# Kernel optimization log

Measured on AMD Instinct MI355X. Metric: run time of the kernel, lower is better.

## Reference

```python
import jax, jax.numpy as jnp
import numpy as np

B, DIM, N, K, NA = 1, 64, 1024, 16, 12
POS_HID = 64
ATTN_HID = 4 * DIM


def setup_inputs() -> dict:
    key = jax.random.key(0)
    ks = jax.random.split(key, 8)
    s = 0.05  # small init scale, mimics xavier magnitude
    return {
        "xyz": jax.random.normal(ks[0], (B, 3, N), jnp.float32),
        "feats": jax.random.normal(ks[1], (B, DIM, N, NA), jnp.float32),
        "anchors": jax.random.normal(ks[2], (NA, 3, 3), jnp.float32),
        "to_qkv": jax.random.normal(ks[3], (3 * DIM, DIM), jnp.float32) * s,
        "pos_mlp1": jax.random.normal(ks[4], (POS_HID, 3), jnp.float32) * s,
        "pos_mlp2": jax.random.normal(ks[5], (DIM, POS_HID), jnp.float32) * s,
        "attn_mlp1": jax.random.normal(ks[6], (ATTN_HID, DIM), jnp.float32) * s,
        "attn_mlp2": jax.random.normal(ks[7], (DIM, ATTN_HID), jnp.float32) * s,
    }


def reference(xyz, feats, anchors, to_qkv, pos_mlp1, pos_mlp2, attn_mlp1, attn_mlp2):
    # --- KNN over points (self included) ---
    pts = jnp.swapaxes(xyz, 1, 2)                      # [B,N,3]
    sq = jnp.sum(pts * pts, axis=-1)                   # [B,N]
    d2 = sq[:, :, None] + sq[:, None, :] - 2.0 * jnp.einsum('bnd,bmd->bnm', pts, pts)
    _, idx = jax.lax.top_k(-d2, K)                     # [B,N,K] nearest indices

    # --- gather helpers (vmapped over batch) ---
    gather3 = jax.vmap(lambda x, i: x[:, i])           # [C,N],[N,K] -> [C,N,K]
    gather4 = jax.vmap(lambda x, i: x[:, i, :])        # [C,N,A],[N,K] -> [C,N,K,A]

    # --- relative positions rotated by anchors ---
    grouped_xyz = gather3(xyz, idx)                    # [B,3,N,K]
    rel = xyz[:, :, :, None] - grouped_xyz             # [B,3,N,K]
    gx = jnp.einsum('aij,bjnk->binka', anchors, rel)   # [B,3,N,K,NA]

    # --- positional embedding MLP ---
    pe = jnp.einsum('ji,binka->bjnka', pos_mlp1, gx)   # [B,POS_HID,N,K,NA]
    pe = jax.nn.relu(pe)
    pe = jnp.einsum('ji,binka->bjnka', pos_mlp2, pe)   # [B,DIM,N,K,NA]

    # --- qkv projection ---
    qkv = jnp.einsum('ji,bina->bjna', to_qkv, feats)   # [B,3*DIM,N,NA]
    q, k, v = jnp.split(qkv, 3, axis=1)                # each [B,DIM,N,NA]

    k_g = gather4(k, idx)                              # [B,DIM,N,K,NA]
    v_g = gather4(v, idx) + pe                         # [B,DIM,N,K,NA]
    qk_rel = q[:, :, :, None, :] - k_g                 # [B,DIM,N,K,NA]

    # --- attention MLP on (qk_rel + pe) ---
    sim = qk_rel + pe
    sim = jnp.einsum('ji,binka->bjnka', attn_mlp1, sim)  # [B,4*DIM,N,K,NA]
    sim = jax.nn.relu(sim)
    sim = jnp.einsum('ji,binka->bjnka', attn_mlp2, sim)  # [B,DIM,N,K,NA]

    # --- per-channel softmax over neighbor axis, aggregate ---
    attn = jax.nn.softmax(sim, axis=-2)
    return jnp.sum(attn * v_g, axis=-2)                # [B,DIM,N,NA]
```

## Files before the change

### kernel.cpp

```cpp
#include <hip/hip_runtime.h>

#define NPTS 1024
#define DIM 64
#define KNN 16
#define NA 12
#define NCOL 192

typedef __attribute__((ext_vector_type(8))) short bf16x8;
typedef __attribute__((ext_vector_type(4))) float f32x4;

static __device__ inline unsigned short f2bfu(float x) {
    __bf16 b = (__bf16)x;
    return __builtin_bit_cast(unsigned short, b);
}
static __device__ inline float bf2f(unsigned short s) {
    return __uint_as_float(((unsigned)s) << 16);
}
static __device__ inline unsigned pk2(float lo, float hi) {
    return (unsigned)f2bfu(lo) | ((unsigned)f2bfu(hi) << 16);
}
static __device__ inline bf16x8 load8_cvt(const float* p) {
    f32x4 u = *(const f32x4*)p;
    f32x4 v = *(const f32x4*)(p + 4);
    bf16x8 r;
    r[0] = (short)f2bfu(u[0]); r[1] = (short)f2bfu(u[1]); r[2] = (short)f2bfu(u[2]); r[3] = (short)f2bfu(u[3]);
    r[4] = (short)f2bfu(v[0]); r[5] = (short)f2bfu(v[1]); r[6] = (short)f2bfu(v[2]); r[7] = (short)f2bfu(v[3]);
    return r;
}

static __device__ inline int swz(int row, int col) {
    return (row << 6) + (col ^ ((row & 7) << 3));
}

__global__ __launch_bounds__(256) void prep_kernel(const float* __restrict__ feats,
                                                   const float* __restrict__ to_qkv,
                                                   float* __restrict__ qkvT,
                                                   unsigned short* __restrict__ pack,
                                                   const float* __restrict__ pos2,
                                                   const float* __restrict__ am1,
                                                   const float* __restrict__ am2,
                                                   const float* __restrict__ xyz,
                                                   int* __restrict__ idxout) {
    __shared__ unsigned short XT[16][72];
    __shared__ float px[NPTS], py[NPTS], pz[NPTS];
    const int b = blockIdx.x;
    const int t = threadIdx.x;
    const int n0 = b * 16;
    const bool do_knn = (b < 256);

    if (b < 72 && t < 64) {
        int s = b;
        int c16p = t & 15, gp = t >> 4;
        const float* src;
        if (s < 8) {
            int nt = s >> 1, kt = s & 1;
            src = pos2 + (nt * 16 + c16p) * 64 + kt * 32 + gp * 8;
        } else if (s < 40) {
            int u = s - 8, hq = u >> 3, nt = (u >> 1) & 3, kt = u & 1;
            src = am1 + (hq * 64 + nt * 16 + c16p) * 64 + kt * 32 + gp * 8;
        } else {
            int u = s - 40, hq = u >> 3, nt = (u >> 1) & 3, kt = u & 1;
            src = am2 + (nt * 16 + c16p) * 256 + hq * 64 + kt * 32 + gp * 8;
        }
        unsigned short* dst = pack + (s * 64 + t) * 8;
        #pragma unroll
        for (int e = 0; e < 8; ++e) dst[e] = f2bfu(src[e]);
    }

    if (do_knn) {
        for (int m = t; m < NPTS; m += 256) {
            px[m] = xyz[m];
            py[m] = xyz[NPTS + m];
            pz[m] = xyz[2 * NPTS + m];
        }
    }
    for (int e = t; e < 16 * 64; e += 256) {
        int c = e & 15, i = e >> 4;
        XT[c][i] = f2bfu(feats[i * (NPTS * NA) + n0 + c]);
    }
    __syncthreads();

    const int lane = t & 63, w = t >> 6, c16 = lane & 15, g = lane >> 4;

    {
        const f32x4 zero4 = {0.f, 0.f, 0.f, 0.f};
        f32x4 acc[3] = {zero4, zero4, zero4};
        #pragma unroll
        for (int kt = 0; kt < 2; ++kt) {
            bf16x8 af = *(const bf16x8*)&XT[c16][kt * 32 + g * 8];
            #pragma unroll
            for (int ni = 0; ni < 3; ++ni) {
                int cd = (w * 3 + ni) * 16 + c16;
                bf16x8 bfr = load8_cvt(to_qkv + cd * 64 + kt * 32 + g * 8);
                acc[ni] = __builtin_amdgcn_mfma_f32_16x16x32_bf16(af, bfr, acc[ni], 0, 0, 0);
            }
        }
        #pragma unroll
        for (int ni = 0; ni < 3; ++ni) {
            int cd = (w * 3 + ni) * 16 + c16;
            int c = cd >> 6, d = cd & 63;
            #pragma unroll
            for (int r = 0; r < 4; ++r) {
                int na = n0 + 4 * g + r;
                qkvT[c * (NPTS * NA * DIM) + na * 64 + d] = acc[ni][r];
            }
        }
    }

    if (do_knn) {
        const int n = b * 4 + w;
        const float xn = px[n], yn = py[n], zn = pz[n];
        const float sqn = xn * xn + yn * yn + zn * zn;
        float dd[16]; int id[16];
        #pragma unroll
        for (int j = 0; j < 16; ++j) {
            int m = j * 64 + lane;
            float xm = px[m], ym = py[m], zm = pz[m];
            float sqm = xm * xm + ym * ym + zm * zm;
            float dot = xn * xm + yn * ym + zn * zm;
            dd[j] = sqn + sqm - 2.f * dot;
            id[j] = m;
        }
        for (int r = 0; r < KNN; ++r) {
            float bd = 1e30f; int bi = 0x7fffffff;
            #pragma unroll
            for (int j = 0; j < 16; ++j)
                if (dd[j] < bd || (dd[j] == bd && id[j] < bi)) { bd = dd[j]; bi = id[j]; }
            #pragma unroll
            for (int mask = 1; mask < 64; mask <<= 1) {
                float od = __shfl_xor(bd, mask);
                int oi = __shfl_xor(bi, mask);
                if (od < bd || (od == bd && oi < bi)) { bd = od; bi = oi; }
            }
            if (lane == 0) idxout[n * KNN + r] = bi;
            #pragma unroll
            for (int j = 0; j < 16; ++j)
                if (id[j] == bi) dd[j] = 1e30f;
        }
    }
}

__global__ __launch_bounds__(512, 4) void attn_main(const float* __restrict__ xyz,
                                                    const float* __restrict__ anchors,
                                                    const float* __restrict__ pos1,
                                                    const unsigned short* __restrict__ pack,
                                                    const float* __restrict__ qT,
                                                    const float* __restrict__ kT,
                                                    const float* __restrict__ vT,
                                                    const int* __restrict__ nn,
                                                    float* __restrict__ out) {
    __shared__ __align__(16) unsigned short XbT[NCOL * 64];
    __shared__ __align__(16) unsigned short HqT[NCOL * 64];
    __shared__ float relb[KNN][3];
    __shared__ float ab[108];
    __shared__ float gbuf[3][NCOL];
    __shared__ int nidx[KNN];

    const int n = blockIdx.x, t = threadIdx.x;
    const int lane = t & 63, wave = t >> 6;
    const int c16 = lane & 15, g = lane >> 4;
    const int mw = wave & 3;
    const int nw = wave >> 2;

    if (t < 108) ab[t] = anchors[t];
    if (t < KNN) {
        int m = nn[n * KNN + t];
        nidx[t] = m;
        relb[t][0] = xyz[n] - xyz[m];
        relb[t][1] = xyz[NPTS + n] - xyz[NPTS + m];
        relb[t][2] = xyz[2 * NPTS + n] - xyz[2 * NPTS + m];
    }
    __syncthreads();

    for (int e = t; e < 3 * NCOL; e += 512) {
        int row = e / NCOL, col = e % NCOL;
        int a = col >> 4, k = col & 15;
        gbuf[row][col] = ab[a * 9 + row * 3 + 0] * relb[k][0]
                       + ab[a * 9 + row * 3 + 1] * relb[k][1]
                       + ab[a * 9 + row * 3 + 2] * relb[k][2];
    }
    __syncthreads();

    {
        const float p10 = pos1[lane * 3 + 0], p11 = pos1[lane * 3 + 1], p12 = pos1[lane * 3 + 2];
        #pragma unroll
        for (int j = 0; j < 24; ++j) {
            int row = wave + 8 * j;
            float p = p10 * gbuf[0][row] + p11 * gbuf[1][row] + p12 * gbuf[2][row];
            XbT[swz(row, lane)] = f2bfu(p > 0.f ? p : 0.f);
        }
    }
    __syncthreads();

    const bf16x8* pk16 = (const bf16x8*)pack;
    const f32x4 zero4 = {0.f, 0.f, 0.f, 0.f};

    f32x4 peacc[6] = {zero4, zero4, zero4, zero4, zero4, zero4};
    #pragma unroll
    for (int kt = 0; kt < 2; ++kt) {
        bf16x8 b0 = pk16[((2 * nw + 0) * 2 + kt) * 64 + lane];
        bf16x8 b1 = pk16[((2 * nw + 1) * 2 + kt) * 64 + lane];
        #pragma unroll
        for (int mi = 0; mi < 3; ++mi) {
            bf16x8 af = *(const bf16x8*)&XbT[swz((mw + 4 * mi) * 16 + c16, kt * 32 + g * 8)];
            peacc[mi * 2 + 0] = __builtin_amdgcn_mfma_f32_16x16x32_bf16(af, b0, peacc[mi * 2 + 0], 0, 0, 0);
            peacc[mi * 2 + 1] = __builtin_amdgcn_mfma_f32_16x16x32_bf16(af, b1, peacc[mi * 2 + 1], 0, 0, 0);
        }
    }

    unsigned vgp[6][2];
    float xreg[6][4];
    {
        const int m0 = nidx[4 * g + 0], m1 = nidx[4 * g + 1];
        const int m2 = nidx[4 * g + 2], m3 = nidx[4 * g + 3];
        #pragma unroll
        for (int mi = 0; mi < 3; ++mi) {
            int a = mw + 4 * mi;
            #pragma unroll
            for (int ni = 0; ni < 2; ++ni) {
                int tile = mi * 2 + ni;
                int d = (2 * nw + ni) * 16 + c16;
                float qv = qT[(n * NA + a) * DIM + d];
                int b0 = (m0 * NA + a) * DIM + d, b1 = (m1 * NA + a) * DIM + d;
                int b2 = (m2 * NA + a) * DIM + d, b3 = (m3 * NA + a) * DIM + d;
                float vg0 = vT[b0] + peacc[tile][0], vg1 = vT[b1] + peacc[tile][1];
                float vg2 = vT[b2] + peacc[tile][2], vg3 = vT[b3] + peacc[tile][3];
                xreg[tile][0] = qv - kT[b0] + peacc[tile][0];
                xreg[tile][1] = qv - kT[b1] + peacc[tile][1];
                xreg[tile][2] = qv - kT[b2] + peacc[tile][2];
                xreg[tile][3] = qv - kT[b3] + peacc[tile][3];
                vgp[tile][0] = pk2(vg0, vg1);
                vgp[tile][1] = pk2(vg2, vg3);
            }
        }
    }
    __syncthreads();
    #pragma unroll
    for (int mi = 0; mi < 3; ++mi)
        #pragma unroll
        for (int ni = 0; ni < 2; ++ni) {
            int tile = mi * 2 + ni;
            int col = (2 * nw + ni) * 16 + c16;
            #pragma unroll
            for (int r = 0; r < 4; ++r)
                XbT[swz((mw + 4 * mi) * 16 + 4 * g + r, col)] = f2bfu(xreg[tile][r]);
        }
    __syncthreads();

    f32x4 sacc[6] = {zero4, zero4, zero4, zero4, zero4, zero4};
    for (int hq = 0; hq < 4; ++hq) {
        f32x4 hacc[6] = {zero4, zero4, zero4, zero4, zero4, zero4};
        #pragma unroll
        for (int kt = 0; kt < 2; ++kt) {
            bf16x8 b0 = pk16[(8 + (hq * 4 + 2 * nw + 0) * 2 + kt) * 64 + lane];
            bf16x8 b1 = pk16[(8 + (hq * 4 + 2 * nw + 1) * 2 + kt) * 64 + lane];
            #pragma unroll
            for (int mi = 0; mi < 3; ++mi) {
                bf16x8 af = *(const bf16x8*)&XbT[swz((mw + 4 * mi) * 16 + c16, kt * 32 + g * 8)];
                hacc[mi * 2 + 0] = __builtin_amdgcn_mfma_f32_16x16x32_bf16(af, b0, hacc[mi * 2 + 0], 0, 0, 0);
                hacc[mi * 2 + 1] = __builtin_amdgcn_mfma_f32_16x16x32_bf16(af, b1, hacc[mi * 2 + 1], 0, 0, 0);
            }
        }
        #pragma unroll
        for (int mi = 0; mi < 3; ++mi)
            #pragma unroll
            for (int ni = 0; ni < 2; ++ni) {
                int tile = mi * 2 + ni;
                int col = (2 * nw + ni) * 16 + c16;
                #pragma unroll
                for (int r = 0; r < 4; ++r)
                    HqT[swz((mw + 4 * mi) * 16 + 4 * g + r, col)] = f2bfu(fmaxf(hacc[tile][r], 0.f));
            }
        __syncthreads();
        #pragma unroll
        for (int kt = 0; kt < 2; ++kt) {
            bf16x8 b0 = pk16[(40 + hq * 8 + (2 * nw + 0) * 2 + kt) * 64 + lane];
            bf16x8 b1 = pk16[(40 + hq * 8 + (2 * nw + 1) * 2 + kt) * 64 + lane];
            #pragma unroll
            for (int mi = 0; mi < 3; ++mi) {
                bf16x8 af = *(const bf16x8*)&HqT[swz((mw + 4 * mi) * 16 + c16, kt * 32 + g * 8)];
                sacc[mi * 2 + 0] = __builtin_amdgcn_mfma_f32_16x16x32_bf16(af, b0, sacc[mi * 2 + 0], 0, 0, 0);
                sacc[mi * 2 + 1] = __builtin_amdgcn_mfma_f32_16x16x32_bf16(af, b1, sacc[mi * 2 + 1], 0, 0, 0);
            }
        }
        __syncthreads();
    }

    #pragma unroll
    for (int mi = 0; mi < 3; ++mi) {
        int a = mw + 4 * mi;
        #pragma unroll
        for (int ni = 0; ni < 2; ++ni) {
            int tile = mi * 2 + ni;
            int d = (2 * nw + ni) * 16 + c16;
            float e0 = __expf(sacc[tile][0]);
            float e1 = __expf(sacc[tile][1]);
            float e2 = __expf(sacc[tile][2]);
            float e3 = __expf(sacc[tile][3]);
            float den = (e0 + e1) + (e2 + e3);
            unsigned v01 = vgp[tile][0], v23 = vgp[tile][1];
            float num = (e0 * bf2f((unsigned short)(v01 & 0xffff)) + e1 * bf2f((unsigned short)(v01 >> 16)))
                      + (e2 * bf2f((unsigned short)(v23 & 0xffff)) + e3 * bf2f((unsigned short)(v23 >> 16)));
            den += __shfl_xor(den, 16); num += __shfl_xor(num, 16);
            den += __shfl_xor(den, 32); num += __shfl_xor(num, 32);
            if (g == 0)
                out[(d * NPTS + n) * NA + a] = num / den;
        }
    }
}

extern "C" void kernel_launch(void* const* d_in, const int* in_sizes, int n_in,
                              void* d_out, int out_size, void* d_ws, size_t ws_size,
                              hipStream_t stream) {
    const float* xyz     = (const float*)d_in[0];
    const float* feats   = (const float*)d_in[1];
    const float* anchors = (const float*)d_in[2];
    const float* to_qkv  = (const float*)d_in[3];
    const float* pos1    = (const float*)d_in[4];
    const float* pos2    = (const float*)d_in[5];
    const float* am1     = (const float*)d_in[6];
    const float* am2     = (const float*)d_in[7];
    float* out = (float*)d_out;

    float* ws = (float*)d_ws;
    const int seg = NPTS * NA * DIM;
    float* qT = ws;
    float* kT = ws + seg;
    float* vT = ws + 2 * seg;
    int* nn = (int*)(ws + 3 * seg);
    unsigned short* pack = (unsigned short*)(ws + 3 * seg + NPTS * KNN);

    prep_kernel<<<768, 256, 0, stream>>>(feats, to_qkv, qT, pack, pos2, am1, am2, xyz, nn);
    attn_main<<<NPTS, 512, 0, stream>>>(xyz, anchors, pos1, pack, qT, kT, vT, nn, out);
}
```

Baseline: 91.50 us.

## Fuse KNN, QKV projection and attention into a single per-point kernel

Merges the prep kernel (KNN, QKV projection, weight packing) into the attention kernel, so each block runs its own KNN in one wave, gathers neighbor features and computes k/v for its 16 neighbors with MFMA instead of reading precomputed q/k/v from global memory. This removes the second launch and the large workspace write and read of qkv. In exchange the k/v projection is recomputed for every neighbor, about 16x redundant, and the weights are converted from fp32 to bf16 on the fly. The swizzled shared layout is replaced by padded rows (XPAD=76), with shared buffers reused for the xyz staging.

```diff
diff --git a/kernel.cpp b/kernel.cpp
--- a/kernel.cpp
+++ b/kernel.cpp
@@ -5,6 +5,7 @@
 #define KNN 16
 #define NA 12
 #define NCOL 192
+#define XPAD 76
 
 typedef __attribute__((ext_vector_type(8))) short bf16x8;
 typedef __attribute__((ext_vector_type(4))) float f32x4;
@@ -28,87 +29,45 @@
     return r;
 }
 
-static __device__ inline int swz(int row, int col) {
-    return (row << 6) + (col ^ ((row & 7) << 3));
-}
-
-__global__ __launch_bounds__(256) void prep_kernel(const float* __restrict__ feats,
-                                                   const float* __restrict__ to_qkv,
-                                                   float* __restrict__ qkvT,
-                                                   unsigned short* __restrict__ pack,
-                                                   const float* __restrict__ pos2,
-                                                   const float* __restrict__ am1,
-                                                   const float* __restrict__ am2,
-                                                   const float* __restrict__ xyz,
-                                                   int* __restrict__ idxout) {
-    __shared__ unsigned short XT[16][72];
-    __shared__ float px[NPTS], py[NPTS], pz[NPTS];
-    const int b = blockIdx.x;
-    const int t = threadIdx.x;
-    const int n0 = b * 16;
-    const bool do_knn = (b < 256);
-
-    if (b < 72 && t < 64) {
-        int s = b;
-        int c16p = t & 15, gp = t >> 4;
-        const float* src;
-        if (s < 8) {
-            int nt = s >> 1, kt = s & 1;
-            src = pos2 + (nt * 16 + c16p) * 64 + kt * 32 + gp * 8;
-        } else if (s < 40) {
-            int u = s - 8, hq = u >> 3, nt = (u >> 1) & 3, kt = u & 1;
-            src = am1 + (hq * 64 + nt * 16 + c16p) * 64 + kt * 32 + gp * 8;
-        } else {
-            int u = s - 40, hq = u >> 3, nt = (u >> 1) & 3, kt = u & 1;
-            src = am2 + (nt * 16 + c16p) * 256 + hq * 64 + kt * 32 + gp * 8;
-        }
-        unsigned short* dst = pack + (s * 64 + t) * 8;
-        #pragma unroll
-        for (int e = 0; e < 8; ++e) dst[e] = f2bfu(src[e]);
-    }
-
-    if (do_knn) {
-        for (int m = t; m < NPTS; m += 256) {
-            px[m] = xyz[m];
-            py[m] = xyz[NPTS + m];
-            pz[m] = xyz[2 * NPTS + m];
-        }
-    }
-    for (int e = t; e < 16 * 64; e += 256) {
-        int c = e & 15, i = e >> 4;
-        XT[c][i] = f2bfu(feats[i * (NPTS * NA) + n0 + c]);
-    }
-    __syncthreads();
-
-    const int lane = t & 63, w = t >> 6, c16 = lane & 15, g = lane >> 4;
-
-    {
-        const f32x4 zero4 = {0.f, 0.f, 0.f, 0.f};
-        f32x4 acc[3] = {zero4, zero4, zero4};
-        #pragma unroll
-        for (int kt = 0; kt < 2; ++kt) {
-            bf16x8 af = *(const bf16x8*)&XT[c16][kt * 32 + g * 8];
-            #pragma unroll
-            for (int ni = 0; ni < 3; ++ni) {
-                int cd = (w * 3 + ni) * 16 + c16;
-                bf16x8 bfr = load8_cvt(to_qkv + cd * 64 + kt * 32 + g * 8);
-                acc[ni] = __builtin_amdgcn_mfma_f32_16x16x32_bf16(af, bfr, acc[ni], 0, 0, 0);
-            }
-        }
-        #pragma unroll
-        for (int ni = 0; ni < 3; ++ni) {
-            int cd = (w * 3 + ni) * 16 + c16;
-            int c = cd >> 6, d = cd & 63;
-            #pragma unroll
-            for (int r = 0; r < 4; ++r) {
-                int na = n0 + 4 * g + r;
-                qkvT[c * (NPTS * NA * DIM) + na * 64 + d] = acc[ni][r];
-            }
-        }
-    }
-
-    if (do_knn) {
-        const int n = b * 4 + w;
+__global__ __launch_bounds__(512, 4) void fused1(const float* __restrict__ xyz,
+                                                 const float* __restrict__ feats,
+                                                 const float* __restrict__ anchors,
+                                                 const float* __restrict__ to_qkv,
+                                                 const float* __restrict__ pos1,
+                                                 const float* __restrict__ pos2,
+                                                 const float* __restrict__ am1,
+                                                 const float* __restrict__ am2,
+                                                 float* __restrict__ out) {
+    __shared__ __align__(16) unsigned short R1[208 * XPAD];
+    __shared__ __align__(16) unsigned short R2[NCOL * XPAD];
+    __shared__ float P1s[192];
+    __shared__ float ab[108];
+    __shared__ float relb[KNN][3];
+    __shared__ int nidx[KNN];
+
+    const int n = blockIdx.x, t = threadIdx.x;
+    const int lane = t & 63, wave = t >> 6;
+    const int c16 = lane & 15, g = lane >> 4;
+    const int mw = wave & 3;
+    const int nw = wave >> 2;
+    const f32x4 zero4 = {0.f, 0.f, 0.f, 0.f};
+
+    float* px = (float*)R2;
+    float* py = px + NPTS;
+    float* pz = py + NPTS;
+    float* gbuf = pz + NPTS;
+    float* qbuf = gbuf + 3 * NCOL;
+
+    for (int m = t; m < NPTS; m += 512) {
+        px[m] = xyz[m];
+        py[m] = xyz[NPTS + m];
+        pz[m] = xyz[2 * NPTS + m];
+    }
+    if (t < 192) P1s[t] = pos1[t];
+    if (t < 108) ab[t] = anchors[t];
+    __syncthreads();
+
+    if (wave == 0) {
         const float xn = px[n], yn = py[n], zn = pz[n];
         const float sqn = xn * xn + yn * yn + zn * zn;
         float dd[16]; int id[16];
@@ -121,6 +80,7 @@
             dd[j] = sqn + sqm - 2.f * dot;
             id[j] = m;
         }
+        int mym = 0;
         for (int r = 0; r < KNN; ++r) {
             float bd = 1e30f; int bi = 0x7fffffff;
             #pragma unroll
@@ -132,108 +92,113 @@
                 int oi = __shfl_xor(bi, mask);
                 if (od < bd || (od == bd && oi < bi)) { bd = od; bi = oi; }
             }
-            if (lane == 0) idxout[n * KNN + r] = bi;
+            if (lane == 0) nidx[r] = bi;
+            if (lane == r) mym = bi;
             #pragma unroll
             for (int j = 0; j < 16; ++j)
                 if (id[j] == bi) dd[j] = 1e30f;
         }
-    }
-}
-
-__global__ __launch_bounds__(512, 4) void attn_main(const float* __restrict__ xyz,
-                                                    const float* __restrict__ anchors,
-                                                    const float* __restrict__ pos1,
-                                                    const unsigned short* __restrict__ pack,
-                                                    const float* __restrict__ qT,
-                                                    const float* __restrict__ kT,
-                                                    const float* __restrict__ vT,
-                                                    const int* __restrict__ nn,
-                                                    float* __restrict__ out) {
-    __shared__ __align__(16) unsigned short XbT[NCOL * 64];
-    __shared__ __align__(16) unsigned short HqT[NCOL * 64];
-    __shared__ float relb[KNN][3];
-    __shared__ float ab[108];
-    __shared__ float gbuf[3][NCOL];
-    __shared__ int nidx[KNN];
-
-    const int n = blockIdx.x, t = threadIdx.x;
-    const int lane = t & 63, wave = t >> 6;
-    const int c16 = lane & 15, g = lane >> 4;
-    const int mw = wave & 3;
-    const int nw = wave >> 2;
-
-    if (t < 108) ab[t] = anchors[t];
-    if (t < KNN) {
-        int m = nn[n * KNN + t];
-        nidx[t] = m;
-        relb[t][0] = xyz[n] - xyz[m];
-        relb[t][1] = xyz[NPTS + n] - xyz[NPTS + m];
-        relb[t][2] = xyz[2 * NPTS + n] - xyz[2 * NPTS + m];
-    }
-    __syncthreads();
-
+        if (lane < KNN) {
+            relb[lane][0] = px[n] - px[mym];
+            relb[lane][1] = py[n] - py[mym];
+            relb[lane][2] = pz[n] - pz[mym];
+        }
+    }
+    __syncthreads();
+
+    for (int e = t; e < 208 * 64; e += 512) {
+        int j = e >> 6, i = e & 63;
+        int m, a;
+        if (j < NCOL) { a = j >> 4; m = nidx[j & 15]; }
+        else          { a = j - NCOL; m = n; if (a >= NA) continue; }
+        R1[j * XPAD + i] = f2bfu(feats[i * (NPTS * NA) + m * NA + a]);
+    }
     for (int e = t; e < 3 * NCOL; e += 512) {
         int row = e / NCOL, col = e % NCOL;
         int a = col >> 4, k = col & 15;
-        gbuf[row][col] = ab[a * 9 + row * 3 + 0] * relb[k][0]
-                       + ab[a * 9 + row * 3 + 1] * relb[k][1]
-                       + ab[a * 9 + row * 3 + 2] * relb[k][2];
+        gbuf[row * NCOL + col] = ab[a * 9 + row * 3 + 0] * relb[k][0]
+                               + ab[a * 9 + row * 3 + 1] * relb[k][1]
+                               + ab[a * 9 + row * 3 + 2] * relb[k][2];
+    }
+    __syncthreads();
+
+    f32x4 kacc[6] = {zero4, zero4, zero4, zero4, zero4, zero4};
+    f32x4 vacc[6] = {zero4, zero4, zero4, zero4, zero4, zero4};
+    #pragma unroll
+    for (int kt = 0; kt < 2; ++kt) {
+        bf16x8 bk0 = load8_cvt(to_qkv + (64 + (2 * nw + 0) * 16 + c16) * 64 + kt * 32 + g * 8);
+        bf16x8 bk1 = load8_cvt(to_qkv + (64 + (2 * nw + 1) * 16 + c16) * 64 + kt * 32 + g * 8);
+        bf16x8 bv0 = load8_cvt(to_qkv + (128 + (2 * nw + 0) * 16 + c16) * 64 + kt * 32 + g * 8);
+        bf16x8 bv1 = load8_cvt(to_qkv + (128 + (2 * nw + 1) * 16 + c16) * 64 + kt * 32 + g * 8);
+        #pragma unroll
+        for (int mi = 0; mi < 3; ++mi) {
+            bf16x8 af = *(const bf16x8*)&R1[((mw + 4 * mi) * 16 + c16) * XPAD + kt * 32 + g * 8];
+            kacc[mi * 2 + 0] = __builtin_amdgcn_mfma_f32_16x16x32_bf16(af, bk0, kacc[mi * 2 + 0], 0, 0, 0);
+            kacc[mi * 2 + 1] = __builtin_amdgcn_mfma_f32_16x16x32_bf16(af, bk1, kacc[mi * 2 + 1], 0, 0, 0);
+            vacc[mi * 2 + 0] = __builtin_amdgcn_mfma_f32_16x16x32_bf16(af, bv0, vacc[mi * 2 + 0], 0, 0, 0);
+            vacc[mi * 2 + 1] = __builtin_amdgcn_mfma_f32_16x16x32_bf16(af, bv1, vacc[mi * 2 + 1], 0, 0, 0);
+        }
+    }
+    if (mw == 0) {
+        f32x4 qacc[2] = {zero4, zero4};
+        #pragma unroll
+        for (int kt = 0; kt < 2; ++kt) {
+            bf16x8 af = *(const bf16x8*)&R1[(NCOL + c16) * XPAD + kt * 32 + g * 8];
+            bf16x8 bq0 = load8_cvt(to_qkv + ((2 * nw + 0) * 16 + c16) * 64 + kt * 32 + g * 8);
+            bf16x8 bq1 = load8_cvt(to_qkv + ((2 * nw + 1) * 16 + c16) * 64 + kt * 32 + g * 8);
+            qacc[0] = __builtin_amdgcn_mfma_f32_16x16x32_bf16(af, bq0, qacc[0], 0, 0, 0);
+            qacc[1] = __builtin_amdgcn_mfma_f32_16x16x32_bf16(af, bq1, qacc[1], 0, 0, 0);
+        }
+        #pragma unroll
+        for (int ni = 0; ni < 2; ++ni)
+            #pragma unroll
+            for (int r = 0; r < 4; ++r) {
+                int a = 4 * g + r;
+                if (a < NA) qbuf[a * 64 + (2 * nw + ni) * 16 + c16] = qacc[ni][r];
+            }
     }
     __syncthreads();
 
     {
-        const float p10 = pos1[lane * 3 + 0], p11 = pos1[lane * 3 + 1], p12 = pos1[lane * 3 + 2];
+        const float p10 = P1s[lane * 3 + 0], p11 = P1s[lane * 3 + 1], p12 = P1s[lane * 3 + 2];
         #pragma unroll
         for (int j = 0; j < 24; ++j) {
-            int row = wave + 8 * j;
-            float p = p10 * gbuf[0][row] + p11 * gbuf[1][row] + p12 * gbuf[2][row];
-            XbT[swz(row, lane)] = f2bfu(p > 0.f ? p : 0.f);
-        }
-    }
-    __syncthreads();
-
-    const bf16x8* pk16 = (const bf16x8*)pack;
-    const f32x4 zero4 = {0.f, 0.f, 0.f, 0.f};
+            int col = wave + 8 * j;
+            float pv = p10 * gbuf[col] + p11 * gbuf[NCOL + col] + p12 * gbuf[2 * NCOL + col];
+            R1[col * XPAD + lane] = f2bfu(pv > 0.f ? pv : 0.f);
+        }
+    }
+    __syncthreads();
 
     f32x4 peacc[6] = {zero4, zero4, zero4, zero4, zero4, zero4};
     #pragma unroll
     for (int kt = 0; kt < 2; ++kt) {
-        bf16x8 b0 = pk16[((2 * nw + 0) * 2 + kt) * 64 + lane];
-        bf16x8 b1 = pk16[((2 * nw + 1) * 2 + kt) * 64 + lane];
+        bf16x8 b0 = load8_cvt(pos2 + ((2 * nw + 0) * 16 + c16) * 64 + kt * 32 + g * 8);
+        bf16x8 b1 = load8_cvt(pos2 + ((2 * nw + 1) * 16 + c16) * 64 + kt * 32 + g * 8);
         #pragma unroll
         for (int mi = 0; mi < 3; ++mi) {
-            bf16x8 af = *(const bf16x8*)&XbT[swz((mw + 4 * mi) * 16 + c16, kt * 32 + g * 8)];
+            bf16x8 af = *(const bf16x8*)&R1[((mw + 4 * mi) * 16 + c16) * XPAD + kt * 32 + g * 8];
             peacc[mi * 2 + 0] = __builtin_amdgcn_mfma_f32_16x16x32_bf16(af, b0, peacc[mi * 2 + 0], 0, 0, 0);
             peacc[mi * 2 + 1] = __builtin_amdgcn_mfma_f32_16x16x32_bf16(af, b1, peacc[mi * 2 + 1], 0, 0, 0);
         }
     }
 
+    float xreg[6][4];
     unsigned vgp[6][2];
-    float xreg[6][4];
-    {
-        const int m0 = nidx[4 * g + 0], m1 = nidx[4 * g + 1];
-        const int m2 = nidx[4 * g + 2], m3 = nidx[4 * g + 3];
-        #pragma unroll
-        for (int mi = 0; mi < 3; ++mi) {
-            int a = mw + 4 * mi;
-            #pragma unroll
-            for (int ni = 0; ni < 2; ++ni) {
-                int tile = mi * 2 + ni;
-                int d = (2 * nw + ni) * 16 + c16;
-                float qv = qT[(n * NA + a) * DIM + d];
-                int b0 = (m0 * NA + a) * DIM + d, b1 = (m1 * NA + a) * DIM + d;
-                int b2 = (m2 * NA + a) * DIM + d, b3 = (m3 * NA + a) * DIM + d;
-                float vg0 = vT[b0] + peacc[tile][0], vg1 = vT[b1] + peacc[tile][1];
-                float vg2 = vT[b2] + peacc[tile][2], vg3 = vT[b3] + peacc[tile][3];
-                xreg[tile][0] = qv - kT[b0] + peacc[tile][0];
-                xreg[tile][1] = qv - kT[b1] + peacc[tile][1];
-                xreg[tile][2] = qv - kT[b2] + peacc[tile][2];
-                xreg[tile][3] = qv - kT[b3] + peacc[tile][3];
-                vgp[tile][0] = pk2(vg0, vg1);
-                vgp[tile][1] = pk2(vg2, vg3);
-            }
-        }
-    }
+    #pragma unroll
+    for (int mi = 0; mi < 3; ++mi)
+        #pragma unroll
+        for (int ni = 0; ni < 2; ++ni) {
+            int tile = mi * 2 + ni;
+            float qv = qbuf[(mw + 4 * mi) * 64 + (2 * nw + ni) * 16 + c16];
+            float vg0 = vacc[tile][0] + peacc[tile][0], vg1 = vacc[tile][1] + peacc[tile][1];
+            float vg2 = vacc[tile][2] + peacc[tile][2], vg3 = vacc[tile][3] + peacc[tile][3];
+            #pragma unroll
+            for (int r = 0; r < 4; ++r)
+                xreg[tile][r] = qv - kacc[tile][r] + peacc[tile][r];
+            vgp[tile][0] = pk2(vg0, vg1);
+            vgp[tile][1] = pk2(vg2, vg3);
+        }
     __syncthreads();
     #pragma unroll
     for (int mi = 0; mi < 3; ++mi)
@@ -243,7 +208,7 @@
             int col = (2 * nw + ni) * 16 + c16;
             #pragma unroll
             for (int r = 0; r < 4; ++r)
-                XbT[swz((mw + 4 * mi) * 16 + 4 * g + r, col)] = f2bfu(xreg[tile][r]);
+                R1[((mw + 4 * mi) * 16 + 4 * g + r) * XPAD + col] = f2bfu(xreg[tile][r]);
         }
     __syncthreads();
 
@@ -252,11 +217,11 @@
         f32x4 hacc[6] = {zero4, zero4, zero4, zero4, zero4, zero4};
         #pragma unroll
         for (int kt = 0; kt < 2; ++kt) {
-            bf16x8 b0 = pk16[(8 + (hq * 4 + 2 * nw + 0) * 2 + kt) * 64 + lane];
-            bf16x8 b1 = pk16[(8 + (hq * 4 + 2 * nw + 1) * 2 + kt) * 64 + lane];
+            bf16x8 b0 = load8_cvt(am1 + (hq * 64 + (2 * nw + 0) * 16 + c16) * 64 + kt * 32 + g * 8);
+            bf16x8 b1 = load8_cvt(am1 + (hq * 64 + (2 * nw + 1) * 16 + c16) * 64 + kt * 32 + g * 8);
             #pragma unroll
             for (int mi = 0; mi < 3; ++mi) {
-                bf16x8 af = *(const bf16x8*)&XbT[swz((mw + 4 * mi) * 16 + c16, kt * 32 + g * 8)];
+                bf16x8 af = *(const bf16x8*)&R1[((mw + 4 * mi) * 16 + c16) * XPAD + kt * 32 + g * 8];
                 hacc[mi * 2 + 0] = __builtin_amdgcn_mfma_f32_16x16x32_bf16(af, b0, hacc[mi * 2 + 0], 0, 0, 0);
                 hacc[mi * 2 + 1] = __builtin_amdgcn_mfma_f32_16x16x32_bf16(af, b1, hacc[mi * 2 + 1], 0, 0, 0);
             }
@@ -269,16 +234,16 @@
                 int col = (2 * nw + ni) * 16 + c16;
                 #pragma unroll
                 for (int r = 0; r < 4; ++r)
-                    HqT[swz((mw + 4 * mi) * 16 + 4 * g + r, col)] = f2bfu(fmaxf(hacc[tile][r], 0.f));
+                    R2[((mw + 4 * mi) * 16 + 4 * g + r) * XPAD + col] = f2bfu(fmaxf(hacc[tile][r], 0.f));
             }
         __syncthreads();
         #pragma unroll
         for (int kt = 0; kt < 2; ++kt) {
-            bf16x8 b0 = pk16[(40 + hq * 8 + (2 * nw + 0) * 2 + kt) * 64 + lane];
-            bf16x8 b1 = pk16[(40 + hq * 8 + (2 * nw + 1) * 2 + kt) * 64 + lane];
+            bf16x8 b0 = load8_cvt(am2 + (((2 * nw + 0) * 16 + c16)) * 256 + hq * 64 + kt * 32 + g * 8);
+            bf16x8 b1 = load8_cvt(am2 + (((2 * nw + 1) * 16 + c16)) * 256 + hq * 64 + kt * 32 + g * 8);
             #pragma unroll
             for (int mi = 0; mi < 3; ++mi) {
-                bf16x8 af = *(const bf16x8*)&HqT[swz((mw + 4 * mi) * 16 + c16, kt * 32 + g * 8)];
+                bf16x8 af = *(const bf16x8*)&R2[((mw + 4 * mi) * 16 + c16) * XPAD + kt * 32 + g * 8];
                 sacc[mi * 2 + 0] = __builtin_amdgcn_mfma_f32_16x16x32_bf16(af, b0, sacc[mi * 2 + 0], 0, 0, 0);
                 sacc[mi * 2 + 1] = __builtin_amdgcn_mfma_f32_16x16x32_bf16(af, b1, sacc[mi * 2 + 1], 0, 0, 0);
             }
@@ -322,14 +287,5 @@
     const float* am2     = (const float*)d_in[7];
     float* out = (float*)d_out;
 
-    float* ws = (float*)d_ws;
-    const int seg = NPTS * NA * DIM;
-    float* qT = ws;
-    float* kT = ws + seg;
-    float* vT = ws + 2 * seg;
-    int* nn = (int*)(ws + 3 * seg);
-    unsigned short* pack = (unsigned short*)(ws + 3 * seg + NPTS * KNN);
-
-    prep_kernel<<<768, 256, 0, stream>>>(feats, to_qkv, qT, pack, pos2, am1, am2, xyz, nn);
-    attn_main<<<NPTS, 512, 0, stream>>>(xyz, anchors, pos1, pack, qT, kT, vT, nn, out);
-}
+    fused1<<<NPTS, 512, 0, stream>>>(xyz, feats, anchors, to_qkv, pos1, pos2, am1, am2, out);
+}
```

Measured after the change: 186.7 us. 104% more time.
